# Kernel optimization log

Measured on AMD Instinct MI355X. Metric: run time of the kernel, lower is better.

Reference implementation:

```python
import jax, jax.numpy as jnp
import numpy as np

B, H, V, T = 1024, 512, 2048, 32  # batch, hidden_size, output_size (vocab), max_len


def setup_inputs() -> dict:
    key = jax.random.key(0)
    ks = jax.random.split(key, 8)
    s = 1.0 / np.sqrt(H)  # torch LSTMCell/Linear init scale
    u = lambda k, shp: jax.random.uniform(k, shp, jnp.float32, -s, s)
    return {
        "encoder_hidden": jax.random.normal(ks[0], (B, H), jnp.float32),
        "encoder_cell": jax.random.normal(ks[1], (B, H), jnp.float32),
        "W_ih": u(ks[2], (4 * H, V)),   # LSTMCell(output_size -> hidden)
        "W_hh": u(ks[3], (4 * H, H)),
        "b_ih": u(ks[4], (4 * H,)),
        "b_hh": u(ks[5], (4 * H,)),
        "W_out": u(ks[6], (V, H)),      # Linear(hidden -> output_size)
        "b_out": u(ks[7], (V,)),
        "init_input": jnp.zeros((1, V), jnp.float32),
        "max_len": T,
        "eos_idx": 0,
    }


def reference(encoder_hidden, encoder_cell, W_ih, W_hh, b_ih, b_hh, W_out, b_out,
              init_input, max_len, eos_idx):
    batch = encoder_hidden.shape[0]
    vocab = W_out.shape[0]
    hid = encoder_hidden.shape[1]

    def lstm_cell(x, h, c):
        gates = x @ W_ih.T + b_ih + h @ W_hh.T + b_hh  # [B, 4H]
        i, f, g, o = jnp.split(gates, 4, axis=1)       # torch gate order i,f,g,o
        c_new = jax.nn.sigmoid(f) * c + jax.nn.sigmoid(i) * jnp.tanh(g)
        h_new = jax.nn.sigmoid(o) * jnp.tanh(c_new)
        return h_new, c_new

    def step(carry, _):
        h, c, x, mask = carry
        h, c = lstm_cell(x, h, c)
        logit = h @ W_out.T + b_out                    # [B, V]
        # eval / non-msg path: hard argmax one-hot
        predict = jax.nn.one_hot(jnp.argmax(logit, axis=1), vocab, dtype=mask.dtype)
        new_mask = mask * (1.0 - predict[:, eos_idx])  # [1, B]
        # embedding is None -> decoder_input = predict
        return (h, c, predict, new_mask), (predict, logit, mask)

    carry0 = (
        encoder_hidden,
        encoder_cell,
        jnp.broadcast_to(init_input, (batch, vocab)),
        jnp.ones((1, batch), jnp.float32),
    )
    _, (predicts, logits, masks) = jax.lax.scan(step, carry0, None, length=max_len)
    return predicts, logits, masks  # [T,B,V], [T,B,V], [T,1,B]
```

## Files before the change

### kernel.cpp

```cpp
#include <hip/hip_runtime.h>
#include <math.h>

#define B_ 1024
#define H_ 512
#define V_ 2048
#define T_ 32
#define G_ 2048
#define KP 1024
#define K3 1536

#define A_SCALE 64.0f
#define B_SCALE 256.0f
#define SCALE_INV (1.0f / (64.0f * 256.0f))

typedef _Float16 f16x8 __attribute__((ext_vector_type(8)));
typedef float f32x4 __attribute__((ext_vector_type(4)));

__device__ __forceinline__ float sigmoidf_(float x) {
    return 1.0f / (1.0f + expf(-x));
}

__device__ __forceinline__ void stage16(const _Float16* g, _Float16* l) {
#if __has_builtin(__builtin_amdgcn_global_load_lds)
    __builtin_amdgcn_global_load_lds(
        (const __attribute__((address_space(1))) void*)g,
        (__attribute__((address_space(3))) void*)l, 16, 0, 0);
#else
    *(uint4*)l = *(const uint4*)g;
#endif
}

__global__ __launch_bounds__(256) void gemm1_fused(
    const _Float16* __restrict__ Hin,
    const _Float16* __restrict__ Wg,
    const float* __restrict__ bsum,
    const float* __restrict__ g0,
    const float* __restrict__ W_ihT,
    const float* __restrict__ W_ih,
    const int* __restrict__ idx,
    float* __restrict__ c,
    _Float16* __restrict__ Hout,
    int t, int modeA)
{
    __shared__ _Float16 As[64 * 32];
    __shared__ _Float16 Bs[64 * 32];
    const int tid = threadIdx.x;
    const int bm  = blockIdx.y * 64;
    const int bnj = blockIdx.x * 16;

    const int r   = tid >> 2;
    const int c16 = tid & 3;
    const int gcB = ((r >> 4) << 9) + bnj + (r & 15);
    const _Float16* aSrc = Hin + (size_t)(bm + r) * KP + c16 * 8;
    const _Float16* bSrc = Wg  + (size_t)gcB * KP + c16 * 8;
    _Float16* aDst = As + tid * 8;
    _Float16* bDst = Bs + tid * 8;

    const int w    = tid >> 6;
    const int lane = tid & 63;
    const int l15  = lane & 15;
    const int kq   = lane >> 4;

    f32x4 acc[4];
#pragma unroll
    for (int q = 0; q < 4; ++q) acc[q] = (f32x4){0.f, 0.f, 0.f, 0.f};

    for (int kk = 0; kk < K3; kk += 32) {
        const int aoff = (kk < 512) ? kk : kk - 512;
        const int boff = (kk < 1024) ? kk : kk - 1024;
        stage16(aSrc + aoff, aDst);
        stage16(bSrc + boff, bDst);
        asm volatile("s_waitcnt vmcnt(0)" ::: "memory");
        __syncthreads();
        f16x8 a = *(const f16x8*)&As[(w * 16 + l15) * 32 + kq * 8];
#pragma unroll
        for (int nt = 0; nt < 4; ++nt) {
            f16x8 b = *(const f16x8*)&Bs[(nt * 16 + l15) * 32 + kq * 8];
            acc[nt] = __builtin_amdgcn_mfma_f32_16x16x32_f16(a, b, acc[nt], 0, 0, 0);
        }
        __syncthreads();
    }

    const int j = bnj + l15;
#pragma unroll
    for (int rg = 0; rg < 4; ++rg) {
        const int row = bm + w * 16 + kq * 4 + rg;
        float xg0, xg1, xg2, xg3;
        if (t == 0) {
            xg0 = g0[j]; xg1 = g0[512 + j]; xg2 = g0[1024 + j]; xg3 = g0[1536 + j];
        } else if (modeA) {
            const float* xr = W_ihT + (size_t)idx[row] * G_;
            xg0 = xr[j]; xg1 = xr[512 + j]; xg2 = xr[1024 + j]; xg3 = xr[1536 + j];
        } else {
            const int v = idx[row];
            xg0 = W_ih[(size_t)(j) * V_ + v];
            xg1 = W_ih[(size_t)(512 + j) * V_ + v];
            xg2 = W_ih[(size_t)(1024 + j) * V_ + v];
            xg3 = W_ih[(size_t)(1536 + j) * V_ + v];
        }
        const float gi = acc[0][rg] * SCALE_INV + bsum[j]        + xg0;
        const float gf = acc[1][rg] * SCALE_INV + bsum[512 + j]  + xg1;
        const float gg = acc[2][rg] * SCALE_INV + bsum[1024 + j] + xg2;
        const float go = acc[3][rg] * SCALE_INV + bsum[1536 + j] + xg3;
        const float co = c[(size_t)row * H_ + j];
        const float cn = sigmoidf_(gf) * co + sigmoidf_(gi) * tanhf(gg);
        const float hn = sigmoidf_(go) * tanhf(cn);
        c[(size_t)row * H_ + j] = cn;
        const float hs = A_SCALE * hn;
        const _Float16 hi = (_Float16)hs;
        const _Float16 lo = (_Float16)(hs - (float)hi);
        Hout[(size_t)row * KP + j] = hi;
        Hout[(size_t)row * KP + 512 + j] = lo;
    }
}

__global__ __launch_bounds__(256) void gemm2_fused(
    const _Float16* __restrict__ Hin,
    const _Float16* __restrict__ Wo,
    const float* __restrict__ b_out,
    float* __restrict__ logits,
    float* __restrict__ pval,
    int* __restrict__ pidx)
{
    __shared__ _Float16 As[64 * 32];
    __shared__ _Float16 Bs[64 * 32];
    const int tid = threadIdx.x;
    const int bm = blockIdx.y * 64;
    const int bn = blockIdx.x * 64;

    const int r   = tid >> 2;
    const int c16 = tid & 3;
    const _Float16* aSrc = Hin + (size_t)(bm + r) * KP + c16 * 8;
    const _Float16* bSrc = Wo  + (size_t)(bn + r) * KP + c16 * 8;
    _Float16* aDst = As + tid * 8;
    _Float16* bDst = Bs + tid * 8;

    const int w    = tid >> 6;
    const int wm   = w & 1;
    const int wn   = w >> 1;
    const int lane = tid & 63;
    const int l15  = lane & 15;
    const int kq   = lane >> 4;

    f32x4 acc[2][2];
#pragma unroll
    for (int i = 0; i < 2; ++i)
#pragma unroll
        for (int k = 0; k < 2; ++k) acc[i][k] = (f32x4){0.f, 0.f, 0.f, 0.f};

    for (int kk = 0; kk < K3; kk += 32) {
        const int aoff = (kk < 512) ? kk : kk - 512;
        const int boff = (kk < 1024) ? kk : kk - 1024;
        stage16(aSrc + aoff, aDst);
        stage16(bSrc + boff, bDst);
        asm volatile("s_waitcnt vmcnt(0)" ::: "memory");
        __syncthreads();
        f16x8 a0 = *(const f16x8*)&As[(wm * 32 + l15) * 32 + kq * 8];
        f16x8 a1 = *(const f16x8*)&As[(wm * 32 + 16 + l15) * 32 + kq * 8];
        f16x8 b0 = *(const f16x8*)&Bs[(wn * 32 + l15) * 32 + kq * 8];
        f16x8 b1 = *(const f16x8*)&Bs[(wn * 32 + 16 + l15) * 32 + kq * 8];
        acc[0][0] = __builtin_amdgcn_mfma_f32_16x16x32_f16(a0, b0, acc[0][0], 0, 0, 0);
        acc[0][1] = __builtin_amdgcn_mfma_f32_16x16x32_f16(a0, b1, acc[0][1], 0, 0, 0);
        acc[1][0] = __builtin_amdgcn_mfma_f32_16x16x32_f16(a1, b0, acc[1][0], 0, 0, 0);
        acc[1][1] = __builtin_amdgcn_mfma_f32_16x16x32_f16(a1, b1, acc[1][1], 0, 0, 0);
        __syncthreads();
    }

    const int cid = blockIdx.x * 2 + wn;
    const int c0  = bn + wn * 32 + l15;
    const int c1  = c0 + 16;
    const float bo0 = b_out[c0];
    const float bo1 = b_out[c1];
#pragma unroll
    for (int mt = 0; mt < 2; ++mt) {
#pragma unroll
        for (int rg = 0; rg < 4; ++rg) {
            const int row = bm + wm * 32 + mt * 16 + kq * 4 + rg;
            const float v0 = acc[mt][0][rg] * SCALE_INV + bo0;
            const float v1 = acc[mt][1][rg] * SCALE_INV + bo1;
            logits[(size_t)row * V_ + c0] = v0;
            logits[(size_t)row * V_ + c1] = v1;
            float bv; int bc;
            if (v1 > v0) { bv = v1; bc = c1; } else { bv = v0; bc = c0; }
#pragma unroll
            for (int off = 1; off < 16; off <<= 1) {
                const float ov = __shfl_xor(bv, off, 64);
                const int   oc = __shfl_xor(bc, off, 64);
                if (ov > bv || (ov == bv && oc < bc)) { bv = ov; bc = oc; }
            }
            if (l15 == 0) { pval[row * 64 + cid] = bv; pidx[row * 64 + cid] = bc; }
        }
    }
}

__global__ __launch_bounds__(256) void finalize_step(
    const float* __restrict__ pval, const int* __restrict__ pidx,
    float* __restrict__ predicts_t, float* __restrict__ masks_t,
    float* __restrict__ mask, int* __restrict__ idx,
    const int* __restrict__ eos_idx)
{
    const int row = blockIdx.x * 256 + threadIdx.x;
    if (row >= B_) return;
    float bv = pval[row * 64];
    int   bc = pidx[row * 64];
    for (int cd = 1; cd < 64; ++cd) {
        const float v = pval[row * 64 + cd];
        if (v > bv) { bv = v; bc = pidx[row * 64 + cd]; }
    }
    idx[row] = bc;
    predicts_t[(size_t)row * V_ + bc] = 1.0f;
    masks_t[row] = mask[row];
    if (bc == *eos_idx) mask[row] = 0.0f;
}

__global__ __launch_bounds__(256) void prep_misc(
    const float* __restrict__ eh, const float* __restrict__ ec,
    const float* __restrict__ b_ih, const float* __restrict__ b_hh,
    _Float16* __restrict__ hA, float* __restrict__ c,
    float* __restrict__ bsum, float* __restrict__ mask)
{
    const int gid = blockIdx.x * 256 + threadIdx.x;
    const int row = gid >> 9;
    const int j   = gid & 511;
    const float x = eh[gid];
    c[gid] = ec[gid];
    const float xs = A_SCALE * x;
    const _Float16 hi = (_Float16)xs;
    const _Float16 lo = (_Float16)(xs - (float)hi);
    hA[(size_t)row * KP + j] = hi;
    hA[(size_t)row * KP + 512 + j] = lo;
    if (gid < G_) bsum[gid] = b_ih[gid] + b_hh[gid];
    if (gid < B_) mask[gid] = 1.0f;
}

__global__ __launch_bounds__(256) void prep_w(
    const float* __restrict__ W_hh, const float* __restrict__ W_out,
    _Float16* __restrict__ Wg, _Float16* __restrict__ Wo)
{
    const int gid = blockIdx.x * 256 + threadIdx.x;
    const int sel = gid >> 20;
    const int i   = gid & 1048575;
    const int n   = i >> 9;
    const int k   = i & 511;
    const float ws = (sel ? W_out[i] : W_hh[i]) * B_SCALE;
    const _Float16 hi = (_Float16)ws;
    const _Float16 lo = (_Float16)(ws - (float)hi);
    _Float16* dst = sel ? Wo : Wg;
    dst[(size_t)n * KP + k] = hi;
    dst[(size_t)n * KP + 512 + k] = lo;
}

__global__ __launch_bounds__(256) void transpose2048(const float* __restrict__ in,
                                                     float* __restrict__ out)
{
    __shared__ float tile[32][33];
    const int bx = blockIdx.x * 32;
    const int by = blockIdx.y * 32;
    const int tx = threadIdx.x & 31;
    const int ty = threadIdx.x >> 5;
#pragma unroll
    for (int i = 0; i < 32; i += 8)
        tile[ty + i][tx] = in[(size_t)(by + ty + i) * V_ + bx + tx];
    __syncthreads();
#pragma unroll
    for (int i = 0; i < 32; i += 8)
        out[(size_t)(bx + ty + i) * G_ + by + tx] = tile[tx][ty + i];
}

__global__ __launch_bounds__(256) void g0_kernel(const float* __restrict__ init_input,
                                                 const float* __restrict__ W_ih,
                                                 float* __restrict__ g0)
{
    const int gc   = blockIdx.x * 4 + (threadIdx.x >> 6);
    const int lane = threadIdx.x & 63;
    float acc = 0.0f;
    for (int v = lane; v < V_; v += 64) acc += init_input[v] * W_ih[(size_t)gc * V_ + v];
#pragma unroll
    for (int off = 32; off > 0; off >>= 1) acc += __shfl_down(acc, off, 64);
    if (lane == 0) g0[gc] = acc;
}

extern "C" void kernel_launch(void* const* d_in, const int* in_sizes, int n_in,
                              void* d_out, int out_size, void* d_ws, size_t ws_size,
                              hipStream_t stream) {
    const float* enc_h      = (const float*)d_in[0];
    const float* enc_c      = (const float*)d_in[1];
    const float* W_ih       = (const float*)d_in[2];
    const float* W_hh       = (const float*)d_in[3];
    const float* b_ih       = (const float*)d_in[4];
    const float* b_hh       = (const float*)d_in[5];
    const float* W_out      = (const float*)d_in[6];
    const float* b_out      = (const float*)d_in[7];
    const float* init_input = (const float*)d_in[8];
    const int*   eos_idx    = (const int*)d_in[10];

    float* out      = (float*)d_out;
    float* predicts = out;
    float* logits   = out + (size_t)T_ * B_ * V_;
    float* masks    = out + 2 * (size_t)T_ * B_ * V_;

    size_t off = 0;
    auto alloc = [&](size_t bytes) {
        void* p = (char*)d_ws + off;
        off += (bytes + 255) & ~(size_t)255;
        return p;
    };
    _Float16* Wg   = (_Float16*)alloc((size_t)G_ * KP * 2);
    _Float16* Wo   = (_Float16*)alloc((size_t)V_ * KP * 2);
    _Float16* hA   = (_Float16*)alloc((size_t)B_ * KP * 2);
    _Float16* hB   = (_Float16*)alloc((size_t)B_ * KP * 2);
    float*    c    = (float*)alloc((size_t)B_ * H_ * 4);
    float*    pval = (float*)alloc((size_t)B_ * 64 * 4);
    int*      pidx = (int*)alloc((size_t)B_ * 64 * 4);
    float*    g0   = (float*)alloc((size_t)G_ * 4);
    float*    bsum = (float*)alloc((size_t)G_ * 4);
    float*    mask = (float*)alloc((size_t)B_ * 4);
    int*      idx  = (int*)alloc((size_t)B_ * 4);
    float*    W_ihT = (float*)((char*)d_ws + off);
    const int modeA = (off + (size_t)V_ * G_ * 4) <= ws_size;

    hipMemsetAsync(predicts, 0, (size_t)T_ * B_ * V_ * sizeof(float), stream);
    prep_misc<<<(B_ * H_) / 256, 256, 0, stream>>>(enc_h, enc_c, b_ih, b_hh, hA, c, bsum, mask);
    prep_w<<<(2 * G_ * H_) / 256, 256, 0, stream>>>(W_hh, W_out, Wg, Wo);
    g0_kernel<<<G_ / 4, 256, 0, stream>>>(init_input, W_ih, g0);
    if (modeA)
        transpose2048<<<dim3(64, 64), 256, 0, stream>>>(W_ih, W_ihT);

    for (int t = 0; t < T_; ++t) {
        const _Float16* hin = (t & 1) ? hB : hA;
        _Float16*      hout = (t & 1) ? hA : hB;
        gemm1_fused<<<dim3(32, 16), 256, 0, stream>>>(
            hin, Wg, bsum, g0, W_ihT, W_ih, idx, c, hout, t, modeA);
        gemm2_fused<<<dim3(32, 16), 256, 0, stream>>>(
            hout, Wo, b_out, logits + (size_t)t * B_ * V_, pval, pidx);
        finalize_step<<<4, 256, 0, stream>>>(
            pval, pidx, predicts + (size_t)t * B_ * V_, masks + (size_t)t * B_,
            mask, idx, eos_idx);
    }
}
```

Baseline: 2.401 ms.

## Double-buffer LDS staging with larger tiles in both GEMMs, parallelize argmax finalize

Both per-step GEMMs now take 64-wide K chunks, double-buffered in LDS. The next chunk's global-to-LDS loads are issued before the current chunk is computed, with a partial vmcnt wait and raw s_barrier. Tiles grow so each wave issues 8 MFMAs per k-slice (128x64 in gemm1, 64x128 in gemm2), which improves operand reuse and halves block counts. The finalize kernel now reduces the 64 partial argmax candidates per row with a wave shuffle instead of a serial loop. The cost is more LDS and registers per block and fewer blocks (256 per GEMM) to fill the GPU.

```diff
diff --git a/kernel.cpp b/kernel.cpp
--- a/kernel.cpp
+++ b/kernel.cpp
@@ -8,6 +8,7 @@
 #define G_ 2048
 #define KP 1024
 #define K3 1536
+#define NC 24
 
 #define A_SCALE 64.0f
 #define B_SCALE 256.0f
@@ -29,6 +30,8 @@
     *(uint4*)l = *(const uint4*)g;
 #endif
 }
+
+__device__ __forceinline__ void wgbar() { asm volatile("s_barrier" ::: "memory"); }
 
 __global__ __launch_bounds__(256) void gemm1_fused(
     const _Float16* __restrict__ Hin,
@@ -42,17 +45,17 @@
     _Float16* __restrict__ Hout,
     int t, int modeA)
 {
-    __shared__ _Float16 As[64 * 32];
-    __shared__ _Float16 Bs[64 * 32];
+    __shared__ _Float16 As[2 * 2 * 128 * 32];
+    __shared__ _Float16 Bs[2 * 2 * 64 * 32];
     const int tid = threadIdx.x;
-    const int bm  = blockIdx.y * 64;
+    const int bm  = blockIdx.y * 128;
     const int bnj = blockIdx.x * 16;
 
     const int r   = tid >> 2;
-    const int c16 = tid & 3;
+    const int cc  = (tid & 3) * 8;
     const int gcB = ((r >> 4) << 9) + bnj + (r & 15);
-    const _Float16* aSrc = Hin + (size_t)(bm + r) * KP + c16 * 8;
-    const _Float16* bSrc = Wg  + (size_t)gcB * KP + c16 * 8;
+    const _Float16* aSrc = Hin + (size_t)(bm + r) * KP + cc;
+    const _Float16* bSrc = Wg  + (size_t)gcB * KP + cc;
     _Float16* aDst = As + tid * 8;
     _Float16* bDst = Bs + tid * 8;
 
@@ -61,56 +64,90 @@
     const int l15  = lane & 15;
     const int kq   = lane >> 4;
 
-    f32x4 acc[4];
-#pragma unroll
-    for (int q = 0; q < 4; ++q) acc[q] = (f32x4){0.f, 0.f, 0.f, 0.f};
-
-    for (int kk = 0; kk < K3; kk += 32) {
+    f32x4 acc[2][4];
+#pragma unroll
+    for (int mt = 0; mt < 2; ++mt)
+#pragma unroll
+        for (int q = 0; q < 4; ++q) acc[mt][q] = (f32x4){0.f, 0.f, 0.f, 0.f};
+
+    auto STAGE = [&](int buf, int ch) {
+        const int kk = ch * 64;
         const int aoff = (kk < 512) ? kk : kk - 512;
         const int boff = (kk < 1024) ? kk : kk - 1024;
-        stage16(aSrc + aoff, aDst);
-        stage16(bSrc + boff, bDst);
-        asm volatile("s_waitcnt vmcnt(0)" ::: "memory");
-        __syncthreads();
-        f16x8 a = *(const f16x8*)&As[(w * 16 + l15) * 32 + kq * 8];
-#pragma unroll
-        for (int nt = 0; nt < 4; ++nt) {
-            f16x8 b = *(const f16x8*)&Bs[(nt * 16 + l15) * 32 + kq * 8];
-            acc[nt] = __builtin_amdgcn_mfma_f32_16x16x32_f16(a, b, acc[nt], 0, 0, 0);
-        }
-        __syncthreads();
+#pragma unroll
+        for (int ks = 0; ks < 2; ++ks) {
+#pragma unroll
+            for (int hh = 0; hh < 2; ++hh)
+                stage16(aSrc + (size_t)hh * 64 * KP + aoff + ks * 32,
+                        aDst + buf * 8192 + ks * 4096 + hh * 2048);
+            stage16(bSrc + boff + ks * 32, bDst + buf * 4096 + ks * 2048);
+        }
+    };
+
+    int cur = 0;
+    STAGE(0, 0);
+    for (int ch = 0; ch < NC; ++ch) {
+        if (ch + 1 < NC) {
+            STAGE(cur ^ 1, ch + 1);
+            asm volatile("s_waitcnt vmcnt(6)" ::: "memory");
+        } else {
+            asm volatile("s_waitcnt vmcnt(0)" ::: "memory");
+        }
+        wgbar();
+#pragma unroll
+        for (int ks = 0; ks < 2; ++ks) {
+            const _Float16* ab = As + cur * 8192 + ks * 4096;
+            const _Float16* bb = Bs + cur * 4096 + ks * 2048;
+            f16x8 a0 = *(const f16x8*)&ab[(w * 32 + l15) * 32 + kq * 8];
+            f16x8 a1 = *(const f16x8*)&ab[(w * 32 + 16 + l15) * 32 + kq * 8];
+#pragma unroll
+            for (int q = 0; q < 4; ++q) {
+                f16x8 b = *(const f16x8*)&bb[(q * 16 + l15) * 32 + kq * 8];
+                acc[0][q] = __builtin_amdgcn_mfma_f32_16x16x32_f16(a0, b, acc[0][q], 0, 0, 0);
+                acc[1][q] = __builtin_amdgcn_mfma_f32_16x16x32_f16(a1, b, acc[1][q], 0, 0, 0);
+            }
+        }
+        wgbar();
+        cur ^= 1;
     }
 
     const int j = bnj + l15;
-#pragma unroll
-    for (int rg = 0; rg < 4; ++rg) {
-        const int row = bm + w * 16 + kq * 4 + rg;
-        float xg0, xg1, xg2, xg3;
-        if (t == 0) {
-            xg0 = g0[j]; xg1 = g0[512 + j]; xg2 = g0[1024 + j]; xg3 = g0[1536 + j];
-        } else if (modeA) {
-            const float* xr = W_ihT + (size_t)idx[row] * G_;
-            xg0 = xr[j]; xg1 = xr[512 + j]; xg2 = xr[1024 + j]; xg3 = xr[1536 + j];
-        } else {
-            const int v = idx[row];
-            xg0 = W_ih[(size_t)(j) * V_ + v];
-            xg1 = W_ih[(size_t)(512 + j) * V_ + v];
-            xg2 = W_ih[(size_t)(1024 + j) * V_ + v];
-            xg3 = W_ih[(size_t)(1536 + j) * V_ + v];
-        }
-        const float gi = acc[0][rg] * SCALE_INV + bsum[j]        + xg0;
-        const float gf = acc[1][rg] * SCALE_INV + bsum[512 + j]  + xg1;
-        const float gg = acc[2][rg] * SCALE_INV + bsum[1024 + j] + xg2;
-        const float go = acc[3][rg] * SCALE_INV + bsum[1536 + j] + xg3;
-        const float co = c[(size_t)row * H_ + j];
-        const float cn = sigmoidf_(gf) * co + sigmoidf_(gi) * tanhf(gg);
-        const float hn = sigmoidf_(go) * tanhf(cn);
-        c[(size_t)row * H_ + j] = cn;
-        const float hs = A_SCALE * hn;
-        const _Float16 hi = (_Float16)hs;
-        const _Float16 lo = (_Float16)(hs - (float)hi);
-        Hout[(size_t)row * KP + j] = hi;
-        Hout[(size_t)row * KP + 512 + j] = lo;
+    const float bs0 = bsum[j];
+    const float bs1 = bsum[512 + j];
+    const float bs2 = bsum[1024 + j];
+    const float bs3 = bsum[1536 + j];
+#pragma unroll
+    for (int mt = 0; mt < 2; ++mt) {
+#pragma unroll
+        for (int rg = 0; rg < 4; ++rg) {
+            const int row = bm + w * 32 + mt * 16 + kq * 4 + rg;
+            float xg0, xg1, xg2, xg3;
+            if (t == 0) {
+                xg0 = g0[j]; xg1 = g0[512 + j]; xg2 = g0[1024 + j]; xg3 = g0[1536 + j];
+            } else if (modeA) {
+                const float* xr = W_ihT + (size_t)idx[row] * G_;
+                xg0 = xr[j]; xg1 = xr[512 + j]; xg2 = xr[1024 + j]; xg3 = xr[1536 + j];
+            } else {
+                const int v = idx[row];
+                xg0 = W_ih[(size_t)(j) * V_ + v];
+                xg1 = W_ih[(size_t)(512 + j) * V_ + v];
+                xg2 = W_ih[(size_t)(1024 + j) * V_ + v];
+                xg3 = W_ih[(size_t)(1536 + j) * V_ + v];
+            }
+            const float gi = acc[mt][0][rg] * SCALE_INV + bs0 + xg0;
+            const float gf = acc[mt][1][rg] * SCALE_INV + bs1 + xg1;
+            const float gg = acc[mt][2][rg] * SCALE_INV + bs2 + xg2;
+            const float go = acc[mt][3][rg] * SCALE_INV + bs3 + xg3;
+            const float co = c[(size_t)row * H_ + j];
+            const float cn = sigmoidf_(gf) * co + sigmoidf_(gi) * tanhf(gg);
+            const float hn = sigmoidf_(go) * tanhf(cn);
+            c[(size_t)row * H_ + j] = cn;
+            const float hs = A_SCALE * hn;
+            const _Float16 hi = (_Float16)hs;
+            const _Float16 lo = (_Float16)(hs - (float)hi);
+            Hout[(size_t)row * KP + j] = hi;
+            Hout[(size_t)row * KP + 512 + j] = lo;
+        }
     }
 }
 
@@ -122,16 +159,16 @@
     float* __restrict__ pval,
     int* __restrict__ pidx)
 {
-    __shared__ _Float16 As[64 * 32];
-    __shared__ _Float16 Bs[64 * 32];
+    __shared__ _Float16 As[2 * 2 * 64 * 32];
+    __shared__ _Float16 Bs[2 * 2 * 128 * 32];
     const int tid = threadIdx.x;
     const int bm = blockIdx.y * 64;
-    const int bn = blockIdx.x * 64;
-
-    const int r   = tid >> 2;
-    const int c16 = tid & 3;
-    const _Float16* aSrc = Hin + (size_t)(bm + r) * KP + c16 * 8;
-    const _Float16* bSrc = Wo  + (size_t)(bn + r) * KP + c16 * 8;
+    const int bn = blockIdx.x * 128;
+
+    const int r  = tid >> 2;
+    const int cc = (tid & 3) * 8;
+    const _Float16* aSrc = Hin + (size_t)(bm + r) * KP + cc;
+    const _Float16* bSrc = Wo  + (size_t)(bn + r) * KP + cc;
     _Float16* aDst = As + tid * 8;
     _Float16* bDst = Bs + tid * 8;
 
@@ -142,35 +179,57 @@
     const int l15  = lane & 15;
     const int kq   = lane >> 4;
 
-    f32x4 acc[2][2];
-#pragma unroll
-    for (int i = 0; i < 2; ++i)
-#pragma unroll
-        for (int k = 0; k < 2; ++k) acc[i][k] = (f32x4){0.f, 0.f, 0.f, 0.f};
-
-    for (int kk = 0; kk < K3; kk += 32) {
+    f32x4 acc[2][4];
+#pragma unroll
+    for (int mt = 0; mt < 2; ++mt)
+#pragma unroll
+        for (int nt = 0; nt < 4; ++nt) acc[mt][nt] = (f32x4){0.f, 0.f, 0.f, 0.f};
+
+    auto STAGE = [&](int buf, int ch) {
+        const int kk = ch * 64;
         const int aoff = (kk < 512) ? kk : kk - 512;
         const int boff = (kk < 1024) ? kk : kk - 1024;
-        stage16(aSrc + aoff, aDst);
-        stage16(bSrc + boff, bDst);
-        asm volatile("s_waitcnt vmcnt(0)" ::: "memory");
-        __syncthreads();
-        f16x8 a0 = *(const f16x8*)&As[(wm * 32 + l15) * 32 + kq * 8];
-        f16x8 a1 = *(const f16x8*)&As[(wm * 32 + 16 + l15) * 32 + kq * 8];
-        f16x8 b0 = *(const f16x8*)&Bs[(wn * 32 + l15) * 32 + kq * 8];
-        f16x8 b1 = *(const f16x8*)&Bs[(wn * 32 + 16 + l15) * 32 + kq * 8];
-        acc[0][0] = __builtin_amdgcn_mfma_f32_16x16x32_f16(a0, b0, acc[0][0], 0, 0, 0);
-        acc[0][1] = __builtin_amdgcn_mfma_f32_16x16x32_f16(a0, b1, acc[0][1], 0, 0, 0);
-        acc[1][0] = __builtin_amdgcn_mfma_f32_16x16x32_f16(a1, b0, acc[1][0], 0, 0, 0);
-        acc[1][1] = __builtin_amdgcn_mfma_f32_16x16x32_f16(a1, b1, acc[1][1], 0, 0, 0);
-        __syncthreads();
-    }
-
-    const int cid = blockIdx.x * 2 + wn;
-    const int c0  = bn + wn * 32 + l15;
-    const int c1  = c0 + 16;
-    const float bo0 = b_out[c0];
-    const float bo1 = b_out[c1];
+#pragma unroll
+        for (int ks = 0; ks < 2; ++ks) {
+            stage16(aSrc + aoff + ks * 32, aDst + buf * 4096 + ks * 2048);
+#pragma unroll
+            for (int hh = 0; hh < 2; ++hh)
+                stage16(bSrc + (size_t)hh * 64 * KP + boff + ks * 32,
+                        bDst + buf * 8192 + ks * 4096 + hh * 2048);
+        }
+    };
+
+    int cur = 0;
+    STAGE(0, 0);
+    for (int ch = 0; ch < NC; ++ch) {
+        if (ch + 1 < NC) {
+            STAGE(cur ^ 1, ch + 1);
+            asm volatile("s_waitcnt vmcnt(6)" ::: "memory");
+        } else {
+            asm volatile("s_waitcnt vmcnt(0)" ::: "memory");
+        }
+        wgbar();
+#pragma unroll
+        for (int ks = 0; ks < 2; ++ks) {
+            const _Float16* ab = As + cur * 4096 + ks * 2048;
+            const _Float16* bb = Bs + cur * 8192 + ks * 4096;
+            f16x8 a0 = *(const f16x8*)&ab[(wm * 32 + l15) * 32 + kq * 8];
+            f16x8 a1 = *(const f16x8*)&ab[(wm * 32 + 16 + l15) * 32 + kq * 8];
+#pragma unroll
+            for (int nt = 0; nt < 4; ++nt) {
+                f16x8 b = *(const f16x8*)&bb[(wn * 64 + nt * 16 + l15) * 32 + kq * 8];
+                acc[0][nt] = __builtin_amdgcn_mfma_f32_16x16x32_f16(a0, b, acc[0][nt], 0, 0, 0);
+                acc[1][nt] = __builtin_amdgcn_mfma_f32_16x16x32_f16(a1, b, acc[1][nt], 0, 0, 0);
+            }
+        }
+        wgbar();
+        cur ^= 1;
+    }
+
+    const int cb = bn + wn * 64;
+    const int c0 = cb + l15, c1 = cb + 16 + l15, c2 = cb + 32 + l15, c3 = cb + 48 + l15;
+    const float bo0 = b_out[c0], bo1 = b_out[c1], bo2 = b_out[c2], bo3 = b_out[c3];
+    const int cid = blockIdx.x * 4 + wn * 2;
 #pragma unroll
     for (int mt = 0; mt < 2; ++mt) {
 #pragma unroll
@@ -178,8 +237,10 @@
             const int row = bm + wm * 32 + mt * 16 + kq * 4 + rg;
             const float v0 = acc[mt][0][rg] * SCALE_INV + bo0;
             const float v1 = acc[mt][1][rg] * SCALE_INV + bo1;
-            logits[(size_t)row * V_ + c0] = v0;
-            logits[(size_t)row * V_ + c1] = v1;
+            const float v2 = acc[mt][2][rg] * SCALE_INV + bo2;
+            const float v3 = acc[mt][3][rg] * SCALE_INV + bo3;
+            float* lrow = logits + (size_t)row * V_;
+            lrow[c0] = v0; lrow[c1] = v1; lrow[c2] = v2; lrow[c3] = v3;
             float bv; int bc;
             if (v1 > v0) { bv = v1; bc = c1; } else { bv = v0; bc = c0; }
 #pragma unroll
@@ -189,6 +250,14 @@
                 if (ov > bv || (ov == bv && oc < bc)) { bv = ov; bc = oc; }
             }
             if (l15 == 0) { pval[row * 64 + cid] = bv; pidx[row * 64 + cid] = bc; }
+            if (v3 > v2) { bv = v3; bc = c3; } else { bv = v2; bc = c2; }
+#pragma unroll
+            for (int off = 1; off < 16; off <<= 1) {
+                const float ov = __shfl_xor(bv, off, 64);
+                const int   oc = __shfl_xor(bc, off, 64);
+                if (ov > bv || (ov == bv && oc < bc)) { bv = ov; bc = oc; }
+            }
+            if (l15 == 0) { pval[row * 64 + cid + 1] = bv; pidx[row * 64 + cid + 1] = bc; }
         }
     }
 }
@@ -199,18 +268,22 @@
     float* __restrict__ mask, int* __restrict__ idx,
     const int* __restrict__ eos_idx)
 {
-    const int row = blockIdx.x * 256 + threadIdx.x;
-    if (row >= B_) return;
-    float bv = pval[row * 64];
-    int   bc = pidx[row * 64];
-    for (int cd = 1; cd < 64; ++cd) {
-        const float v = pval[row * 64 + cd];
-        if (v > bv) { bv = v; bc = pidx[row * 64 + cd]; }
-    }
-    idx[row] = bc;
-    predicts_t[(size_t)row * V_ + bc] = 1.0f;
-    masks_t[row] = mask[row];
-    if (bc == *eos_idx) mask[row] = 0.0f;
+    const int row  = blockIdx.x * 4 + (threadIdx.x >> 6);
+    const int lane = threadIdx.x & 63;
+    float bv = pval[row * 64 + lane];
+    int   bc = pidx[row * 64 + lane];
+#pragma unroll
+    for (int off = 1; off < 64; off <<= 1) {
+        const float ov = __shfl_xor(bv, off, 64);
+        const int   oc = __shfl_xor(bc, off, 64);
+        if (ov > bv || (ov == bv && oc < bc)) { bv = ov; bc = oc; }
+    }
+    if (lane == 0) {
+        idx[row] = bc;
+        predicts_t[(size_t)row * V_ + bc] = 1.0f;
+        masks_t[row] = mask[row];
+        if (bc == *eos_idx) mask[row] = 0.0f;
+    }
 }
 
 __global__ __launch_bounds__(256) void prep_misc(
@@ -329,11 +402,11 @@
     for (int t = 0; t < T_; ++t) {
         const _Float16* hin = (t & 1) ? hB : hA;
         _Float16*      hout = (t & 1) ? hA : hB;
-        gemm1_fused<<<dim3(32, 16), 256, 0, stream>>>(
+        gemm1_fused<<<dim3(32, 8), 256, 0, stream>>>(
             hin, Wg, bsum, g0, W_ihT, W_ih, idx, c, hout, t, modeA);
-        gemm2_fused<<<dim3(32, 16), 256, 0, stream>>>(
+        gemm2_fused<<<dim3(16, 16), 256, 0, stream>>>(
             hout, Wo, b_out, logits + (size_t)t * B_ * V_, pval, pidx);
-        finalize_step<<<4, 256, 0, stream>>>(
+        finalize_step<<<256, 256, 0, stream>>>(
             pval, pidx, predicts + (size_t)t * B_ * V_, masks + (size_t)t * B_,
             mask, idx, eos_idx);
     }
```

Measured after the change: 2.255 ms. -6.1%, faster.
